# Kernel tuning notes

Hardware: AMD Instinct MI355X
Metric: run time of the kernel (lower is better)

Reference implementation:

```python
import jax, jax.numpy as jnp
import numpy as np

B, S, D, H, HD = 1, 4096, 512, 8, 64
FF = 2048
ROT = 32          # rotary dim (RotaryEmbedding(dim=32))
THETA = 10000.0
EPS = 1e-5


def setup_inputs() -> dict:
    key = jax.random.key(0)
    ks = jax.random.split(key, 10)
    s = 0.02
    return {
        "x": jax.random.normal(ks[0], (B, S, D), jnp.float32),
        "gammas": jnp.ones((2,), jnp.float32),
        "betas": jnp.zeros((2,), jnp.float32),
        "wq": jax.random.normal(ks[1], (D, D), jnp.float32) * s,
        "wk": jax.random.normal(ks[2], (D, D), jnp.float32) * s,
        "wv": jax.random.normal(ks[3], (D, D), jnp.float32) * s,
        "wo": jax.random.normal(ks[4], (D, D), jnp.float32) * s,
        "bo": jnp.zeros((D,), jnp.float32),
        "w1": jax.random.normal(ks[5], (D, FF), jnp.float32) * s,
        "b1": jnp.zeros((FF,), jnp.float32),
        "w2": jax.random.normal(ks[6], (FF, D), jnp.float32) * s,
        "b2": jnp.zeros((D,), jnp.float32),
        "mask": jax.random.randint(ks[7], (B, 1, 1, S), 0, 2, jnp.int32),
    }


def _ln(x):  # LayerNorm, no affine (elementwise_affine=False)
    m = x.mean(-1, keepdims=True)
    v = ((x - m) ** 2).mean(-1, keepdims=True)
    return (x - m) / jnp.sqrt(v + EPS)


def _rope_tables(seq_len, dtype):
    inv_freq = 1.0 / (THETA ** (jnp.arange(0, ROT, 2, dtype=jnp.float32) / ROT))
    freqs = jnp.arange(seq_len, dtype=jnp.float32)[:, None] * inv_freq[None, :]  # (S, ROT/2)
    freqs = jnp.repeat(freqs, 2, axis=-1)  # interleaved: f0,f0,f1,f1,... (S, ROT)
    return jnp.cos(freqs).astype(dtype), jnp.sin(freqs).astype(dtype)


def _apply_rope(t, cos, sin):
    # t: (B,H,S,HD); rotate first ROT dims with interleaved pairs (lucidrains)
    tr, tp = t[..., :ROT], t[..., ROT:]
    x1, x2 = tr[..., 0::2], tr[..., 1::2]
    rot = jnp.stack((-x2, x1), axis=-1).reshape(tr.shape)
    return jnp.concatenate([tr * cos + rot * sin, tp], axis=-1)


def reference(x, gammas, betas, wq, wk, wv, wo, bo, w1, b1, w2, b2, mask):
    # --- attention block ---
    res = x
    h = _ln(x)
    h = gammas[0] * h + betas[0]  # FiLM
    q = (h @ wq).reshape(B, S, H, HD).transpose(0, 2, 1, 3)
    k = (h @ wk).reshape(B, S, H, HD).transpose(0, 2, 1, 3)
    v = (h @ wv).reshape(B, S, H, HD).transpose(0, 2, 1, 3)
    cos, sin = _rope_tables(S, x.dtype)
    q = _apply_rope(q, cos, sin)
    k = _apply_rope(k, cos, sin)
    score = jnp.einsum("bhqd,bhkd->bhqk", q, k) / jnp.sqrt(jnp.asarray(HD, x.dtype))
    score = jnp.where(mask == 0, jnp.asarray(-1e9, x.dtype), score)
    attn = jax.nn.softmax(score, axis=-1)
    out = jnp.einsum("bhqk,bhkd->bhqd", attn, v)
    out = out.transpose(0, 2, 1, 3).reshape(B, S, D)
    x = res + (out @ wo + bo)
    # --- FFN block ---
    res = x
    h = _ln(x)
    h = gammas[1] * h + betas[1]
    h = jax.nn.gelu(h @ w1 + b1, approximate=False) @ w2 + b2
    return res + h
```

## Files before the change

### kernel.cpp

```cpp
#include <hip/hip_runtime.h>
#include <math.h>

constexpr int SEQ  = 4096;
constexpr int DIM  = 512;
constexpr int NH   = 8;
constexpr int HDIM = 64;
constexpr int FFD  = 2048;
constexpr int KSPLIT = 3;

typedef unsigned short u16;
typedef __attribute__((ext_vector_type(8))) short bf16x8;
typedef __attribute__((ext_vector_type(4))) float f32x4;
typedef __attribute__((ext_vector_type(8))) unsigned short u16x8;

#define LOG2E      1.4426950408889634f
#define QSCALE     (0.125f * LOG2E)
#define MASK_OFF   (-1.4427e9f)

static __device__ __forceinline__ u16 f2bf(float x) {
    union { float f; unsigned int u; } v; v.f = x;
    unsigned int r = v.u + 0x7fff + ((v.u >> 16) & 1);
    return (u16)(r >> 16);
}
static __device__ __forceinline__ float bf2f(u16 h) {
    union { unsigned int u; float f; } v; v.u = ((unsigned int)h) << 16;
    return v.f;
}
static __device__ __forceinline__ unsigned int cvtpk(float lo, float hi) {
    unsigned int r;
    asm volatile("v_cvt_pk_bf16_f32 %0, %1, %2" : "=v"(r) : "v"(lo), "v"(hi));
    return r;
}
static __device__ __forceinline__ float exp2f_fast(float x) {
    float r; asm volatile("v_exp_f32 %0, %1" : "=v"(r) : "v"(x)); return r;
}
static __device__ __forceinline__ void gload_lds16(const void* g, void* l) {
    __builtin_amdgcn_global_load_lds(
        (const __attribute__((address_space(1))) unsigned int*)g,
        (__attribute__((address_space(3))) unsigned int*)l, 16, 0, 0);
}

__global__ void prep_kernel(const float* __restrict__ x, u16* __restrict__ h1,
                            const float* __restrict__ gammas, const float* __restrict__ betas,
                            const float* __restrict__ wq, const float* __restrict__ wk,
                            const float* __restrict__ wv, const float* __restrict__ wo,
                            const float* __restrict__ w1, const float* __restrict__ w2,
                            u16* __restrict__ wqkvT, u16* __restrict__ woT,
                            u16* __restrict__ w1T, u16* __restrict__ w2T,
                            const int* __restrict__ mask, float* __restrict__ maskc,
                            int* __restrict__ invidx, int* __restrict__ nkp,
                            float* __restrict__ ct, float* __restrict__ st) {
    __shared__ float smem[1056];
    int b = blockIdx.x;
    int t = threadIdx.x;
    if (b < SEQ / 4) {
        int wv_ = t >> 6, lane = t & 63;
        int row = b * 4 + wv_;
        const float* xr = x + (size_t)row * DIM + lane * 8;
        float4 a0 = *(const float4*)xr;
        float4 a1 = *(const float4*)(xr + 4);
        float f[8] = {a0.x, a0.y, a0.z, a0.w, a1.x, a1.y, a1.z, a1.w};
        float s = 0.f, qs = 0.f;
#pragma unroll
        for (int i = 0; i < 8; i++) { s += f[i]; qs += f[i] * f[i]; }
#pragma unroll
        for (int o = 1; o < 64; o <<= 1) {
            s  += __shfl_xor(s, o, 64);
            qs += __shfl_xor(qs, o, 64);
        }
        float mean = s / DIM;
        float var  = qs / DIM - mean * mean;
        float rstd = rsqrtf(var + 1e-5f);
        float g = gammas[0], be = betas[0];
        u16x8 res;
#pragma unroll
        for (int i = 0; i < 8; i += 2) {
            unsigned int pk = cvtpk(g * ((f[i] - mean) * rstd) + be,
                                    g * ((f[i + 1] - mean) * rstd) + be);
            res[i]     = (u16)(pk & 0xffff);
            res[i + 1] = (u16)(pk >> 16);
        }
        *(u16x8*)(h1 + (size_t)row * DIM + lane * 8) = res;
        return;
    }
    b -= SEQ / 4;
    if (b < 1) {
        __shared__ int cnt[256];
        int base = t * 16;
        int loc[16]; int c = 0;
#pragma unroll
        for (int i = 0; i < 16; i++) { loc[i] = mask[base + i]; c += (loc[i] != 0); }
        cnt[t] = c;
        __syncthreads();
        for (int o = 1; o < 256; o <<= 1) {
            int v = (t >= o) ? cnt[t - o] : 0;
            __syncthreads();
            cnt[t] += v;
            __syncthreads();
        }
        int pos = cnt[t] - c;
        int total = cnt[255];
#pragma unroll
        for (int i = 0; i < 16; i++)
            invidx[base + i] = loc[i] ? pos++ : -1;
#pragma unroll
        for (int i = 0; i < 16; i++)
            maskc[base + i] = (base + i < total) ? 0.0f : MASK_OFF;
        if (t == 0) *nkp = total;
        return;
    }
    b -= 1;
    if (b < 256) {
        int idx = b * 256 + t;
        int s = idx >> 4, i = idx & 15;
        float invf = expf(-(float)i * (9.2103403719761836f / 16.0f));
        float freq = (float)s * invf;
        ct[idx] = cosf(freq);
        st[idx] = sinf(freq);
        return;
    }
    b -= 256;
    const float* src; u16* dst; int K, N; float scale = 1.f;
    if (b < 256)       { src = wq; dst = wqkvT;            K = 512;  N = 512; scale = QSCALE; }
    else if (b < 512)  { src = wk; dst = wqkvT + 512*512;  K = 512;  N = 512; b -= 256; }
    else if (b < 768)  { src = wv; dst = wqkvT + 1024*512; K = 512;  N = 512; b -= 512; }
    else if (b < 1024) { src = wo; dst = woT;              K = 512;  N = 512; b -= 768; }
    else if (b < 2048) { src = w1; dst = w1T;              K = 512;  N = 2048; b -= 1024; }
    else               { src = w2; dst = w2T;              K = 2048; N = 512;  b -= 2048; }
    float (*tile)[33] = (float(*)[33])smem;
    int tiles_x = N / 32;
    int n0 = (b % tiles_x) * 32, k0 = (b / tiles_x) * 32;
    int tx = t & 31, ty = t >> 5;
#pragma unroll
    for (int i = 0; i < 4; i++) {
        int kk = ty + i * 8;
        tile[kk][tx] = src[(size_t)(k0 + kk) * N + n0 + tx];
    }
    __syncthreads();
#pragma unroll
    for (int i = 0; i < 4; i++) {
        int nn = ty + i * 8;
        dst[(size_t)(n0 + nn) * K + k0 + tx] = f2bf(scale * tile[tx][nn]);
    }
}

__global__ void ln_bf16_kernel(const u16* __restrict__ x, u16* __restrict__ out,
                               const float* __restrict__ gammas, const float* __restrict__ betas,
                               int gi) {
    int t = threadIdx.x;
    int wv_ = t >> 6, lane = t & 63;
    int row = blockIdx.x * 4 + wv_;
    u16x8 v = *(const u16x8*)(x + (size_t)row * DIM + lane * 8);
    float f[8];
    float s = 0.f, qs = 0.f;
#pragma unroll
    for (int i = 0; i < 8; i++) { f[i] = bf2f(v[i]); s += f[i]; qs += f[i] * f[i]; }
#pragma unroll
    for (int o = 1; o < 64; o <<= 1) {
        s  += __shfl_xor(s, o, 64);
        qs += __shfl_xor(qs, o, 64);
    }
    float mean = s / DIM;
    float var  = qs / DIM - mean * mean;
    float rstd = rsqrtf(var + 1e-5f);
    float g = gammas[gi], be = betas[gi];
    u16x8 res;
#pragma unroll
    for (int i = 0; i < 8; i += 2) {
        unsigned int pk = cvtpk(g * ((f[i] - mean) * rstd) + be,
                                g * ((f[i + 1] - mean) * rstd) + be);
        res[i]     = (u16)(pk & 0xffff);
        res[i + 1] = (u16)(pk >> 16);
    }
    *(u16x8*)(out + (size_t)row * DIM + lane * 8) = res;
}

constexpr int FLAG_BF16 = 1, FLAG_GELU = 2, FLAG_SPLIT = 4, FLAG_ROPE = 8, FLAG_RESID_BF16 = 16;

template<int MF>
__global__ __launch_bounds__(256) void gemm_bf16(
    const u16* __restrict__ A, const u16* __restrict__ WT,
    const float* __restrict__ bias, const void* __restrict__ resid,
    void* __restrict__ Cq, int M, int N, int K, int flags)
{
    constexpr int BM = MF * 64;
    __shared__ __align__(16) u16 At[2][BM * 128];
    __shared__ __align__(16) u16 Bt[2][64 * 128];
    const int t = threadIdx.x, lane = t & 63, w = t >> 6;
    const int n0 = blockIdx.x * 64, m0 = blockIdx.y * BM;
    const int l15 = lane & 15, l4 = lane >> 4;

    f32x4 acc[MF][4];
#pragma unroll
    for (int m = 0; m < MF; m++)
#pragma unroll
        for (int n = 0; n < 4; n++) acc[m][n] = (f32x4){0.f, 0.f, 0.f, 0.f};

    auto stage = [&](int buf, int k0) {
#pragma unroll
        for (int i = 0; i < MF * 4; i++) {
            int c = (w * MF * 4 + i) * 64 + lane;
            int r = c >> 4, jj = (c & 15) ^ (r & 7);
            gload_lds16(A + (size_t)(m0 + r) * K + k0 + jj * 8,
                        (char*)At[buf] + (w * MF * 4 + i) * 1024);
        }
#pragma unroll
        for (int i = 0; i < 4; i++) {
            int c = (w * 4 + i) * 64 + lane;
            int r = c >> 4, jj = (c & 15) ^ (r & 7);
            gload_lds16(WT + (size_t)(n0 + r) * K + k0 + jj * 8,
                        (char*)Bt[buf] + (w * 4 + i) * 1024);
        }
    };

    const int NT = K / 128;
    stage(0, 0);
    for (int ti = 0; ti < NT; ti++) {
        const int cur = ti & 1;
        asm volatile("s_waitcnt vmcnt(0)" ::: "memory");
        __syncthreads();
        if (ti + 1 < NT) stage(cur ^ 1, (ti + 1) * 128);
        __builtin_amdgcn_s_setprio(1);
#pragma unroll
        for (int kk = 0; kk < 4; kk++) {
            bf16x8 af[MF], bfr[4];
#pragma unroll
            for (int m = 0; m < MF; m++) {
                int row = w * MF * 16 + m * 16 + l15;
                af[m] = *(bf16x8*)((char*)At[cur] + row * 256 +
                                   ((kk * 64 + l4 * 16) ^ ((row & 7) << 4)));
            }
#pragma unroll
            for (int n = 0; n < 4; n++) {
                int row = n * 16 + l15;
                bfr[n] = *(bf16x8*)((char*)Bt[cur] + row * 256 +
                                    ((kk * 64 + l4 * 16) ^ ((row & 7) << 4)));
            }
#pragma unroll
            for (int m = 0; m < MF; m++)
#pragma unroll
                for (int n = 0; n < 4; n++)
                    acc[m][n] = __builtin_amdgcn_mfma_f32_16x16x32_bf16(
                        af[m], bfr[n], acc[m][n], 0, 0, 0);
        }
        __builtin_amdgcn_s_setprio(0);
    }

#pragma unroll
    for (int m = 0; m < MF; m++)
#pragma unroll
        for (int rr = 0; rr < 4; rr++) {
            int row = m0 + w * MF * 16 + m * 16 + l4 * 4 + rr;
#pragma unroll
            for (int n = 0; n < 4; n++) {
                int colg = n0 + n * 16 + l15;
                float cv = acc[m][n][rr];
                if (bias) cv += bias[colg];
                if (flags & FLAG_GELU) cv = 0.5f * cv * (1.0f + erff(cv * 0.70710678118f));
                if (resid) {
                    if (flags & FLAG_RESID_BF16)
                        cv += bf2f(((const u16*)resid)[(size_t)row * N + colg]);
                    else
                        cv += ((const float*)resid)[(size_t)row * N + colg];
                }
                if (flags & FLAG_BF16) {
                    ((u16*)Cq)[(size_t)row * N + colg] = f2bf(cv);
                } else {
                    ((float*)Cq)[(size_t)row * N + colg] = cv;
                }
            }
        }
}

__global__ __launch_bounds__(256, 3) void gemm_qkv(
    const u16* __restrict__ A, const u16* __restrict__ WT,
    void* __restrict__ Cq, void* __restrict__ Ck, void* __restrict__ Cv,
    const float* __restrict__ ct, const float* __restrict__ st,
    const int* __restrict__ invidx,
    int M, int N, int K)
{
    __shared__ __align__(16) u16 At[2][64 * 64];
    __shared__ __align__(16) u16 Bt[2][128 * 64];
    const int t = threadIdx.x, lane = t & 63, w = t >> 6;
    const int wm = w >> 1, wn = w & 1;
    const int n0 = blockIdx.x * 128, m0 = blockIdx.y * 64;
    const int l15 = lane & 15, l4 = lane >> 4;

    f32x4 acc[2][4];
#pragma unroll
    for (int m = 0; m < 2; m++)
#pragma unroll
        for (int n = 0; n < 4; n++) acc[m][n] = (f32x4){0.f, 0.f, 0.f, 0.f};

    auto stage = [&](int buf, int k0) {
#pragma unroll
        for (int i = 0; i < 2; i++) {
            int c = (w * 2 + i) * 64 + lane;
            int r = c >> 3, j = (c & 7) ^ (r & 7);
            gload_lds16(A + (size_t)(m0 + r) * K + k0 + j * 8,
                        (char*)At[buf] + (w * 2 + i) * 1024);
        }
#pragma unroll
        for (int i = 0; i < 4; i++) {
            int c = (w * 4 + i) * 64 + lane;
            int r = c >> 3, j = (c & 7) ^ (r & 7);
            gload_lds16(WT + (size_t)(n0 + r) * K + k0 + j * 8,
                        (char*)Bt[buf] + (w * 4 + i) * 1024);
        }
    };

    const int NT = K / 64;
    stage(0, 0);
    for (int ti = 0; ti < NT; ti++) {
        const int cur = ti & 1;
        asm volatile("s_waitcnt vmcnt(0)" ::: "memory");
        __syncthreads();
        if (ti + 1 < NT) stage(cur ^ 1, (ti + 1) * 64);
        __builtin_amdgcn_s_setprio(1);
#pragma unroll
        for (int kk = 0; kk < 2; kk++) {
            bf16x8 af[2], bfr[4];
#pragma unroll
            for (int m = 0; m < 2; m++) {
                int row = wm * 32 + m * 16 + l15;
                af[m] = *(bf16x8*)((char*)At[cur] + row * 128 +
                                   ((kk * 64 + l4 * 16) ^ ((row & 7) << 4)));
            }
#pragma unroll
            for (int n = 0; n < 4; n++) {
                int row = wn * 64 + n * 16 + l15;
                bfr[n] = *(bf16x8*)((char*)Bt[cur] + row * 128 +
                                    ((kk * 64 + l4 * 16) ^ ((row & 7) << 4)));
            }
#pragma unroll
            for (int m = 0; m < 2; m++)
#pragma unroll
                for (int n = 0; n < 4; n++)
                    acc[m][n] = __builtin_amdgcn_mfma_f32_16x16x32_bf16(
                        af[m], bfr[n], acc[m][n], 0, 0, 0);
        }
        __builtin_amdgcn_s_setprio(0);
    }

    const int which = (n0 + wn * 64) >> 9;
#pragma unroll
    for (int m = 0; m < 2; m++)
#pragma unroll
        for (int rr = 0; rr < 4; rr++) {
            int row = m0 + wm * 32 + m * 16 + l4 * 4 + rr;
            int orow = (which > 0) ? invidx[row] : row;
#pragma unroll
            for (int n = 0; n < 4; n++) {
                int colg = n0 + wn * 64 + n * 16 + l15;
                float cv = acc[m][n][rr];
                if (which < 2 && n < 2) {
                    float partner = __shfl_xor(cv, 1, 64);
                    int i = (n * 16 + l15) >> 1;
                    float cc = ct[row * 16 + i], ss = st[row * 16 + i];
                    cv = (l15 & 1) ? (cv * cc + partner * ss) : (cv * cc - partner * ss);
                }
                if (orow >= 0) {
                    u16* dst = which == 0 ? (u16*)Cq : which == 1 ? (u16*)Ck : (u16*)Cv;
                    dst[(size_t)orow * 512 + (colg & 511)] = f2bf(cv);
                }
            }
        }
}

__global__ __launch_bounds__(256) void gemm128(
    const u16* __restrict__ A, const u16* __restrict__ WT,
    const float* __restrict__ bias,
    void* __restrict__ Cq,
    int M, int N, int K, int flags)
{
    __shared__ __align__(16) u16 At[2][128 * 64];
    __shared__ __align__(16) u16 Bt[2][128 * 64];
    const int t = threadIdx.x, lane = t & 63, w = t >> 6;
    const int wm = w >> 1, wn = w & 1;
    const int n0 = blockIdx.x * 128, m0 = blockIdx.y * 128;
    const int l15 = lane & 15, l4 = lane >> 4;

    f32x4 acc[4][4];
#pragma unroll
    for (int m = 0; m < 4; m++)
#pragma unroll
        for (int n = 0; n < 4; n++) acc[m][n] = (f32x4){0.f, 0.f, 0.f, 0.f};

    auto stage = [&](int buf, int k0) {
#pragma unroll
        for (int i = 0; i < 4; i++) {
            int c = (w * 4 + i) * 64 + lane;
            int r = c >> 3, j = (c & 7) ^ (r & 7);
            gload_lds16(A + (size_t)(m0 + r) * K + k0 + j * 8,
                        (char*)At[buf] + (w * 4 + i) * 1024);
            gload_lds16(WT + (size_t)(n0 + r) * K + k0 + j * 8,
                        (char*)Bt[buf] + (w * 4 + i) * 1024);
        }
    };

    const int NT = K / 64;
    stage(0, 0);
    for (int ti = 0; ti < NT; ti++) {
        const int cur = ti & 1;
        asm volatile("s_waitcnt vmcnt(0)" ::: "memory");
        __syncthreads();
        if (ti + 1 < NT) stage(cur ^ 1, (ti + 1) * 64);
        __builtin_amdgcn_s_setprio(1);
#pragma unroll
        for (int kk = 0; kk < 2; kk++) {
            bf16x8 af[4], bfr[4];
#pragma unroll
            for (int m = 0; m < 4; m++) {
                int row = wm * 64 + m * 16 + l15;
                af[m] = *(bf16x8*)((char*)At[cur] + row * 128 +
                                   ((kk * 64 + l4 * 16) ^ ((row & 7) << 4)));
            }
#pragma unroll
            for (int n = 0; n < 4; n++) {
                int row = wn * 64 + n * 16 + l15;
                bfr[n] = *(bf16x8*)((char*)Bt[cur] + row * 128 +
                                    ((kk * 64 + l4 * 16) ^ ((row & 7) << 4)));
            }
#pragma unroll
            for (int m = 0; m < 4; m++)
#pragma unroll
                for (int n = 0; n < 4; n++)
                    acc[m][n] = __builtin_amdgcn_mfma_f32_16x16x32_bf16(
                        af[m], bfr[n], acc[m][n], 0, 0, 0);
        }
        __builtin_amdgcn_s_setprio(0);
    }

#pragma unroll
    for (int m = 0; m < 4; m++)
#pragma unroll
        for (int rr = 0; rr < 4; rr++) {
            int row = m0 + wm * 64 + m * 16 + l4 * 4 + rr;
#pragma unroll
            for (int n = 0; n < 4; n++) {
                int colg = n0 + wn * 64 + n * 16 + l15;
                float cv = acc[m][n][rr];
                if (bias) cv += bias[colg];
                if (flags & FLAG_GELU) cv = 0.5f * cv * (1.0f + erff(cv * 0.70710678118f));
                ((u16*)Cq)[(size_t)row * N + colg] = f2bf(cv);
            }
        }
}

__global__ void transpose_c(const u16* __restrict__ vc, const int* __restrict__ nkp,
                            u16* __restrict__ vTc) {
    int nk = *nkp;
    int s0 = blockIdx.x * 64;
    if (s0 >= ((nk + 63) & ~63)) return;
    __shared__ __align__(16) u16 tile[64][80];
    int h = blockIdx.y;
    int t = threadIdx.x;
#pragma unroll
    for (int p = 0; p < 2; p++) {
        int c = p * 256 + t;
        int r = c >> 3, j = c & 7;
        u16x8 vv = {};
        if (s0 + r < nk)
            vv = *(const u16x8*)(vc + (size_t)(s0 + r) * DIM + h * HDIM + j * 8);
        *(u16x8*)&tile[r][j * 8] = vv;
    }
    __syncthreads();
#pragma unroll
    for (int p = 0; p < 2; p++) {
        int c = p * 256 + t;
        int d = c >> 3, j = c & 7;
        u16x8 vv;
#pragma unroll
        for (int i = 0; i < 8; i++) vv[i] = tile[j * 8 + i][d];
        *(u16x8*)(vTc + ((size_t)h * HDIM + d) * SEQ + s0 + j * 8) = vv;
    }
}

__global__ __launch_bounds__(256, 3) void fattn_kernel(
    const u16* __restrict__ q, const u16* __restrict__ k,
    const u16* __restrict__ vT, const float* __restrict__ maskc,
    const int* __restrict__ nkp,
    u16* __restrict__ Opart, float* __restrict__ lpart)
{
    __shared__ __align__(16) u16 k_s[2][64 * 64];
    __shared__ __align__(16) u16 vt_s[2][64 * 64];
    __shared__ __align__(16) u16 p_s[4][32 * 64];

    const int t = threadIdx.x;
    const int lane = t & 63;
    const int w = t >> 6;
    const int h = blockIdx.x;
    const int q0 = blockIdx.y * 128;
    const int split = blockIdx.z;
    const int nk = *nkp;
    const int ntiles = (nk + 63) >> 6;
    const int tstart = (split * ntiles) / 3;
    const int tend   = ((split + 1) * ntiles) / 3;
    const int l15 = lane & 15, g = lane >> 4;

    bf16x8 qf[2][2];
#pragma unroll
    for (int qh = 0; qh < 2; qh++) {
        const u16* qrow = q + (size_t)(q0 + w * 32 + qh * 16 + l15) * DIM + h * HDIM;
        qf[qh][0] = *(const bf16x8*)(qrow + g * 8);
        qf[qh][1] = *(const bf16x8*)(qrow + g * 8 + 32);
    }

    const bf16x8 ones = (bf16x8){16256, 16256, 16256, 16256, 16256, 16256, 16256, 16256};

    f32x4 O[2][4];
    f32x4 lacc[2];
#pragma unroll
    for (int qh = 0; qh < 2; qh++) {
#pragma unroll
        for (int dt = 0; dt < 4; dt++) O[qh][dt] = (f32x4){0.f, 0.f, 0.f, 0.f};
        lacc[qh] = (f32x4){0.f, 0.f, 0.f, 0.f};
    }

    char* pbase = (char*)p_s[w];
    const int psw = (l15 & 7) << 4;

    auto stage = [&](int buf, int kb2) {
#pragma unroll
        for (int i = 0; i < 2; i++) {
            int c = (w * 2 + i) * 64 + lane;
            int r = c >> 3, j = (c & 7) ^ (r & 7);
            gload_lds16(k + (size_t)(kb2 + r) * DIM + h * HDIM + j * 8,
                        (char*)k_s + buf * 8192 + (w * 2 + i) * 1024);
            gload_lds16(vT + ((size_t)h * HDIM + r) * SEQ + kb2 + j * 8,
                        (char*)vt_s + buf * 8192 + (w * 2 + i) * 1024);
        }
    };

    if (tstart < tend) stage(0, tstart * 64);
    for (int ti = tstart; ti < tend; ti++) {
        const int cur = (ti - tstart) & 1;
        const int kb = ti * 64;
        asm volatile("s_waitcnt vmcnt(0)" ::: "memory");
        __syncthreads();
        if (ti + 1 < tend) stage(cur ^ 1, kb + 64);

        char* kcur = (char*)k_s + cur * 8192;
        char* vcur = (char*)vt_s + cur * 8192;

        f32x4 sacc[2][4];
        __builtin_amdgcn_s_setprio(1);
#pragma unroll
        for (int kt = 0; kt < 4; kt++) {
            int key = kt * 16 + l15;
            int ksw = (key & 7) << 4;
            char* kbase = kcur + key * 128;
            bf16x8 a0 = *(bf16x8*)(kbase + ((g * 16)      ^ ksw));
            bf16x8 a1 = *(bf16x8*)(kbase + ((g * 16 + 64) ^ ksw));
#pragma unroll
            for (int qh = 0; qh < 2; qh++) {
                f32x4 z = (f32x4){0.f, 0.f, 0.f, 0.f};
                z = __builtin_amdgcn_mfma_f32_16x16x32_bf16(a0, qf[qh][0], z, 0, 0, 0);
                z = __builtin_amdgcn_mfma_f32_16x16x32_bf16(a1, qf[qh][1], z, 0, 0, 0);
                sacc[qh][kt] = z;
            }
        }
        __builtin_amdgcn_s_setprio(0);

        const bool haspad = (ti == ntiles - 1);
        if (!haspad) {
#pragma unroll
            for (int qh = 0; qh < 2; qh++)
#pragma unroll
                for (int kt = 0; kt < 4; kt++) {
                    float p0 = exp2f_fast(sacc[qh][kt][0]);
                    float p1 = exp2f_fast(sacc[qh][kt][1]);
                    float p2 = exp2f_fast(sacc[qh][kt][2]);
                    float p3 = exp2f_fast(sacc[qh][kt][3]);
                    uint2 pk;
                    pk.x = cvtpk(p0, p1);
                    pk.y = cvtpk(p2, p3);
                    int colb = (kt * 16 + g * 4) * 2;
                    *(uint2*)(pbase + (qh * 16 + l15) * 128 + (colb ^ psw)) = pk;
                }
        } else {
            float4 mf4[4];
#pragma unroll
            for (int kt = 0; kt < 4; kt++)
                mf4[kt] = *(const float4*)(maskc + kb + kt * 16 + g * 4);
#pragma unroll
            for (int qh = 0; qh < 2; qh++)
#pragma unroll
                for (int kt = 0; kt < 4; kt++) {
                    float p0 = exp2f_fast(sacc[qh][kt][0] + mf4[kt].x);
                    float p1 = exp2f_fast(sacc[qh][kt][1] + mf4[kt].y);
                    float p2 = exp2f_fast(sacc[qh][kt][2] + mf4[kt].z);
                    float p3 = exp2f_fast(sacc[qh][kt][3] + mf4[kt].w);
                    uint2 pk;
                    pk.x = cvtpk(p0, p1);
                    pk.y = cvtpk(p2, p3);
                    int colb = (kt * 16 + g * 4) * 2;
                    *(uint2*)(pbase + (qh * 16 + l15) * 128 + (colb ^ psw)) = pk;
                }
        }

        __builtin_amdgcn_s_setprio(1);
#pragma unroll
        for (int h2 = 0; h2 < 2; h2++) {
            bf16x8 pb[2];
#pragma unroll
            for (int qh = 0; qh < 2; qh++)
                pb[qh] = *(bf16x8*)(pbase + (qh * 16 + l15) * 128 +
                                    (((h2 * 4 + g) * 16) ^ psw));
#pragma unroll
            for (int dt = 0; dt < 4; dt++) {
                int d = dt * 16 + l15;
                bf16x8 va = *(bf16x8*)(vcur + d * 128 +
                                       (((h2 * 4 + g) * 16) ^ ((d & 7) << 4)));
#pragma unroll
                for (int qh = 0; qh < 2; qh++)
                    O[qh][dt] = __builtin_amdgcn_mfma_f32_16x16x32_bf16(
                        va, pb[qh], O[qh][dt], 0, 0, 0);
            }
#pragma unroll
            for (int qh = 0; qh < 2; qh++)
                lacc[qh] = __builtin_amdgcn_mfma_f32_16x16x32_bf16(
                    ones, pb[qh], lacc[qh], 0, 0, 0);
        }
        __builtin_amdgcn_s_setprio(0);
    }

#pragma unroll
    for (int qh = 0; qh < 2; qh++) {
        float lrun = lacc[qh][0];
        int row = q0 + w * 32 + qh * 16 + l15;
        u16* orow = Opart + (size_t)split * SEQ * DIM + (size_t)row * DIM + h * HDIM;
#pragma unroll
        for (int dt = 0; dt < 4; dt++)
#pragma unroll
            for (int r = 0; r < 4; r += 2) {
                unsigned int pk = cvtpk(O[qh][dt][r], O[qh][dt][r + 1]);
                *(unsigned int*)(orow + dt * 16 + 4 * g + r) = pk;
            }
        if (g == 0)
            lpart[((size_t)split * NH + h) * SEQ + row] = lrun;
    }
}

__global__ void attn_combine(const u16* __restrict__ Opart, const float* __restrict__ lpart,
                             u16* __restrict__ out) {
    int t = threadIdx.x;
    int row = blockIdx.x * 4 + (t >> 6);
    int col = (t & 63) * 8;
    int h = col >> 6;
    float l = lpart[(size_t)h * SEQ + row]
            + lpart[((size_t)NH + h) * SEQ + row]
            + lpart[((size_t)2 * NH + h) * SEQ + row];
    float inv = 1.0f / l;
    const size_t SD = (size_t)SEQ * DIM;
    const u16* base = Opart + (size_t)row * DIM + col;
    u16x8 ua = *(const u16x8*)(base);
    u16x8 ub = *(const u16x8*)(base + SD);
    u16x8 uc = *(const u16x8*)(base + 2 * SD);
    u16x8 res;
#pragma unroll
    for (int j = 0; j < 8; j += 2) {
        float o0 = bf2f(ua[j])     + bf2f(ub[j])     + bf2f(uc[j]);
        float o1 = bf2f(ua[j + 1]) + bf2f(ub[j + 1]) + bf2f(uc[j + 1]);
        unsigned int pk = cvtpk(o0 * inv, o1 * inv);
        res[j]     = (u16)(pk & 0xffff);
        res[j + 1] = (u16)(pk >> 16);
    }
    *(u16x8*)(out + (size_t)row * DIM + col) = res;
}

extern "C" void kernel_launch(void* const* d_in, const int* in_sizes, int n_in,
                              void* d_out, int out_size, void* d_ws, size_t ws_size,
                              hipStream_t stream) {
    const float* x      = (const float*)d_in[0];
    const float* gammas = (const float*)d_in[1];
    const float* betas  = (const float*)d_in[2];
    const float* wq     = (const float*)d_in[3];
    const float* wk     = (const float*)d_in[4];
    const float* wv     = (const float*)d_in[5];
    const float* wo     = (const float*)d_in[6];
    const float* bo     = (const float*)d_in[7];
    const float* w1     = (const float*)d_in[8];
    const float* b1     = (const float*)d_in[9];
    const float* w2     = (const float*)d_in[10];
    const float* b2     = (const float*)d_in[11];
    const int*   mask   = (const int*)d_in[12];
    float* out = (float*)d_out;

    char* wsb = (char*)d_ws;
    u16*   h1b   = (u16*)(wsb + 0);
    u16*   kc    = (u16*)(wsb + (4ull  << 20));
    u16*   vc    = (u16*)(wsb + (8ull  << 20));
    u16*   vTc   = (u16*)(wsb + (12ull << 20));
    u16*   qb    = (u16*)(wsb + (16ull << 20));
    u16*   Opart = (u16*)(wsb + (20ull << 20));
    u16*   x2b   = (u16*)(wsb + (20ull << 20));
    u16*   wqkvT = (u16*)(wsb + (32ull << 20));
    u16*   woT   = wqkvT + 1536 * 512;
    u16*   w1T   = woT   + 512 * 512;
    u16*   w2T   = w1T   + 2048 * 512;
    float* maskc = (float*)(wsb + (38ull << 20));
    int*   invidx= (int*)(wsb + (38ull << 20) + (64 << 10));
    int*   nkp   = (int*)(wsb + (38ull << 20) + (128 << 10));
    float* ct    = (float*)(wsb + (39ull << 20));
    float* st    = ct + 65536;
    float* lpart = (float*)(wsb + (40ull << 20));
    u16*   f1b   = h1b;
    u16*   h2b   = qb;
    u16*   attnb = h1b;

    prep_kernel<<<SEQ / 4 + 1 + 256 + 3072, 256, 0, stream>>>(
        x, h1b, gammas, betas, wq, wk, wv, wo, w1, w2,
        wqkvT, woT, w1T, w2T, mask, maskc, invidx, nkp, ct, st);
    gemm_qkv<<<dim3(1536 / 128, SEQ / 64), 256, 0, stream>>>(
        h1b, wqkvT, qb, kc, vc, ct, st, invidx, SEQ, 1536, DIM);
    transpose_c<<<dim3(SEQ / 64, NH), 256, 0, stream>>>(vc, nkp, vTc);
    fattn_kernel<<<dim3(NH, SEQ / 128, KSPLIT), 256, 0, stream>>>(
        qb, kc, vTc, maskc, nkp, Opart, lpart);
    attn_combine<<<SEQ / 4, 256, 0, stream>>>(Opart, lpart, attnb);
    gemm_bf16<1><<<dim3(DIM / 64, SEQ / 64), 256, 0, stream>>>(
        attnb, woT, bo, (const void*)x, x2b, SEQ, DIM, DIM, FLAG_BF16);
    ln_bf16_kernel<<<SEQ / 4, 256, 0, stream>>>(x2b, h2b, gammas, betas, 1);
    gemm128<<<dim3(FFD / 128, SEQ / 128), 256, 0, stream>>>(
        h2b, w1T, b1, f1b, SEQ, FFD, DIM, FLAG_BF16 | FLAG_GELU);
    gemm_bf16<1><<<dim3(DIM / 64, SEQ / 64), 256, 0, stream>>>(
        f1b, w2T, b2, (const void*)x2b, out, SEQ, DIM, FFD, FLAG_RESID_BF16);
}
```

Baseline: 140.5 us.

## Split W2 FFN GEMM along K into four partials plus combine kernel

```diff
diff --git a/kernel.cpp b/kernel.cpp
--- a/kernel.cpp
+++ b/kernel.cpp
@@ -447,6 +447,110 @@
         }
 }
 
+__global__ __launch_bounds__(256) void gemm_w2split(
+    const u16* __restrict__ A, const u16* __restrict__ WT,
+    u16* __restrict__ p0, u16* __restrict__ p1,
+    u16* __restrict__ p2, u16* __restrict__ p3,
+    int M, int N, int K)
+{
+    __shared__ __align__(16) u16 At[2][128 * 64];
+    __shared__ __align__(16) u16 Bt[2][128 * 64];
+    const int t = threadIdx.x, lane = t & 63, w = t >> 6;
+    const int wm = w >> 1, wn = w & 1;
+    const int n0 = blockIdx.x * 128, m0 = blockIdx.y * 128;
+    const int z = blockIdx.z;
+    const int kbase = z * (K / 4);
+    const int l15 = lane & 15, l4 = lane >> 4;
+
+    f32x4 acc[4][4];
+#pragma unroll
+    for (int m = 0; m < 4; m++)
+#pragma unroll
+        for (int n = 0; n < 4; n++) acc[m][n] = (f32x4){0.f, 0.f, 0.f, 0.f};
+
+    auto stage = [&](int buf, int k0) {
+#pragma unroll
+        for (int i = 0; i < 4; i++) {
+            int c = (w * 4 + i) * 64 + lane;
+            int r = c >> 3, j = (c & 7) ^ (r & 7);
+            gload_lds16(A + (size_t)(m0 + r) * K + k0 + j * 8,
+                        (char*)At[buf] + (w * 4 + i) * 1024);
+            gload_lds16(WT + (size_t)(n0 + r) * K + k0 + j * 8,
+                        (char*)Bt[buf] + (w * 4 + i) * 1024);
+        }
+    };
+
+    const int NT = (K / 4) / 64;
+    stage(0, kbase);
+    for (int ti = 0; ti < NT; ti++) {
+        const int cur = ti & 1;
+        asm volatile("s_waitcnt vmcnt(0)" ::: "memory");
+        __syncthreads();
+        if (ti + 1 < NT) stage(cur ^ 1, kbase + (ti + 1) * 64);
+        __builtin_amdgcn_s_setprio(1);
+#pragma unroll
+        for (int kk = 0; kk < 2; kk++) {
+            bf16x8 af[4], bfr[4];
+#pragma unroll
+            for (int m = 0; m < 4; m++) {
+                int row = wm * 64 + m * 16 + l15;
+                af[m] = *(bf16x8*)((char*)At[cur] + row * 128 +
+                                   ((kk * 64 + l4 * 16) ^ ((row & 7) << 4)));
+            }
+#pragma unroll
+            for (int n = 0; n < 4; n++) {
+                int row = wn * 64 + n * 16 + l15;
+                bfr[n] = *(bf16x8*)((char*)Bt[cur] + row * 128 +
+                                    ((kk * 64 + l4 * 16) ^ ((row & 7) << 4)));
+            }
+#pragma unroll
+            for (int m = 0; m < 4; m++)
+#pragma unroll
+                for (int n = 0; n < 4; n++)
+                    acc[m][n] = __builtin_amdgcn_mfma_f32_16x16x32_bf16(
+                        af[m], bfr[n], acc[m][n], 0, 0, 0);
+        }
+        __builtin_amdgcn_s_setprio(0);
+    }
+
+    u16* pz = (z == 0) ? p0 : (z == 1) ? p1 : (z == 2) ? p2 : p3;
+#pragma unroll
+    for (int m = 0; m < 4; m++)
+#pragma unroll
+        for (int rr = 0; rr < 4; rr++) {
+            int row = m0 + wm * 64 + m * 16 + l4 * 4 + rr;
+#pragma unroll
+            for (int n = 0; n < 4; n++) {
+                int colg = n0 + wn * 64 + n * 16 + l15;
+                pz[(size_t)row * N + colg] = f2bf(acc[m][n][rr]);
+            }
+        }
+}
+
+__global__ void w2_combine(const u16* __restrict__ p0, const u16* __restrict__ p1,
+                           const u16* __restrict__ p2, const u16* __restrict__ p3,
+                           const u16* __restrict__ x2b, const float* __restrict__ b2,
+                           float* __restrict__ out) {
+    int t = threadIdx.x;
+    int row = blockIdx.x * 4 + (t >> 6);
+    int col = (t & 63) * 8;
+    size_t off = (size_t)row * DIM + col;
+    u16x8 a = *(const u16x8*)(p0 + off);
+    u16x8 b = *(const u16x8*)(p1 + off);
+    u16x8 c = *(const u16x8*)(p2 + off);
+    u16x8 d = *(const u16x8*)(p3 + off);
+    u16x8 xr = *(const u16x8*)(x2b + off);
+    float4 bb0 = *(const float4*)(b2 + col);
+    float4 bb1 = *(const float4*)(b2 + col + 4);
+    float bias[8] = {bb0.x, bb0.y, bb0.z, bb0.w, bb1.x, bb1.y, bb1.z, bb1.w};
+    float res[8];
+#pragma unroll
+    for (int j = 0; j < 8; j++)
+        res[j] = bf2f(xr[j]) + bf2f(a[j]) + bf2f(b[j]) + bf2f(c[j]) + bf2f(d[j]) + bias[j];
+    *(float4*)(out + off)     = (float4){res[0], res[1], res[2], res[3]};
+    *(float4*)(out + off + 4) = (float4){res[4], res[5], res[6], res[7]};
+}
+
 __global__ void transpose_c(const u16* __restrict__ vc, const int* __restrict__ nkp,
                             u16* __restrict__ vTc) {
     int nk = *nkp;
@@ -705,6 +809,10 @@
     float* ct    = (float*)(wsb + (39ull << 20));
     float* st    = ct + 65536;
     float* lpart = (float*)(wsb + (40ull << 20));
+    u16*   wp0   = (u16*)(wsb + (24ull << 20));
+    u16*   wp1   = (u16*)(wsb + (28ull << 20));
+    u16*   wp2   = (u16*)(wsb + (16ull << 20));
+    u16*   wp3   = (u16*)(wsb + (41ull << 20));
     u16*   f1b   = h1b;
     u16*   h2b   = qb;
     u16*   attnb = h1b;
@@ -723,6 +831,7 @@
     ln_bf16_kernel<<<SEQ / 4, 256, 0, stream>>>(x2b, h2b, gammas, betas, 1);
     gemm128<<<dim3(FFD / 128, SEQ / 128), 256, 0, stream>>>(
         h2b, w1T, b1, f1b, SEQ, FFD, DIM, FLAG_BF16 | FLAG_GELU);
-    gemm_bf16<1><<<dim3(DIM / 64, SEQ / 64), 256, 0, stream>>>(
-        f1b, w2T, b2, (const void*)x2b, out, SEQ, DIM, FFD, FLAG_RESID_BF16);
-}
+    gemm_w2split<<<dim3(DIM / 128, SEQ / 128, 4), 256, 0, stream>>>(
+        f1b, w2T, wp0, wp1, wp2, wp3, SEQ, DIM, FFD);
+    w2_combine<<<SEQ / 4, 256, 0, stream>>>(wp0, wp1, wp2, wp3, x2b, b2, out);
+}
```

Result: faster. 133.7 us (-4.8%).
